# Optimization experiments

Measured on AMD Instinct MI355X. Metric: run time of the kernel, lower is better.

Reference implementation:

```python
import jax, jax.numpy as jnp
import numpy as np

K = 3  # Chebyshev order
B, T, N, FIN, HID = 2, 12, 8192, 8, 16


def cheb_basis(L, X, k):
    # X: [B, N, F] -> stacked Chebyshev polynomials T_0..T_{k-1}: [k, B, N, F]
    T0 = X
    T1 = jnp.einsum('nm,bmf->bnf', L, X)
    Ts = [T0, T1]
    for _ in range(k - 2):
        Ts.append(2.0 * jnp.einsum('nm,bmf->bnf', L, Ts[-1]) - Ts[-2])
    return jnp.stack(Ts)


def setup_inputs() -> dict:
    key = jax.random.key(0)
    ks = jax.random.split(key, 6)
    X = jax.random.normal(ks[0], (B, T, N, FIN), jnp.float32)
    # scaled so spectral radius ~1, like a rescaled Laplacian (keeps Cheb recursion stable)
    L = jax.random.normal(ks[1], (N, N), jnp.float32) * np.float32(1.0 / np.sqrt(N))
    H = jnp.zeros((T, B, N, HID), jnp.float32)
    C = jnp.zeros((T, B, N, HID), jnp.float32)
    sx = np.float32(1.0 / np.sqrt(FIN * K))
    sh = np.float32(1.0 / np.sqrt(HID * K))
    # per-timestep GConvLSTMCore weights; gate order [i, f, c, o]
    Wx = jax.random.normal(ks[2], (T, 4, K, FIN, HID), jnp.float32) * sx
    Wh = jax.random.normal(ks[3], (T, 4, K, HID, HID), jnp.float32) * sh
    bx = jnp.zeros((T, 4, HID), jnp.float32)
    bh = jnp.zeros((T, 4, HID), jnp.float32)
    # peephole weights, order [w_c_i, w_c_f, w_c_o] (glorot init)
    wc = jax.random.normal(ks[4], (T, 3, HID), jnp.float32) * np.float32(0.3)
    # gate biases [b_i, b_f, b_c, b_o] (zeros init per _set_parameters)
    bg = jnp.zeros((T, 4, HID), jnp.float32)
    return dict(X=X, L=L, H=H, C=C, Wx=Wx, Wh=Wh, bx=bx, bh=bh, wc=wc, bg=bg)


def reference(X, L, H, C, Wx, Wh, bx, bh, wc, bg):
    # GConvLSTMCell forward (dropout=0 / eval): per-timestep GConvLSTMCore with its own weights.
    h0, c0 = H[0], C[0]
    Xt = jnp.transpose(X, (1, 0, 2, 3))  # [T, B, N, FIN]

    def step(carry, xs):
        h, c = carry
        x_t, Wx_t, Wh_t, bx_t, bh_t, wc_t, bg_t = xs
        Tx = cheb_basis(L, x_t, K)           # [K, B, N, FIN]
        Th = cheb_basis(L, h, K)             # [K, B, N, HID]
        # fused 4-gate ChebConv: conv_x_*(X,L) + conv_h_*(H,L) incl. conv biases
        pre = (jnp.einsum('kbnf,gkfh->gbnh', Tx, Wx_t) + bx_t[:, None, None, :]
               + jnp.einsum('kbnf,gkfh->gbnh', Th, Wh_t) + bh_t[:, None, None, :])
        i = jax.nn.sigmoid(pre[0] + wc_t[0] * c + bg_t[0])
        f = jax.nn.sigmoid(pre[1] + wc_t[1] * c + bg_t[1])
        c_new = f * c + i * jnp.tanh(pre[2] + bg_t[2])
        o = jax.nn.sigmoid(pre[3] + wc_t[2] * c_new + bg_t[3])  # uses UPDATED cell state
        h_new = o * jnp.tanh(c_new)
        return (h_new, c_new), (h_new, c_new)

    (_, _), (hs, cs) = jax.lax.scan(step, (h0, c0), (Xt, Wx, Wh, bx, bh, wc, bg))
    out = jnp.transpose(hs, (1, 0, 2, 3))  # [B, T, N, HID]
    return out, hs, cs
```

## Files before the change

kernel.cpp:

```cpp
#include <hip/hip_runtime.h>
#include <hip/hip_bf16.h>

#define N_ 8192
#define T_ 12
#define B_ 2
#define FIN_ 8
#define HID_ 16
#define CGSZ 131072

typedef short s8v __attribute__((ext_vector_type(8)));
typedef float f4v __attribute__((ext_vector_type(4)));

__device__ __forceinline__ float sigmoidf_(float x){ return 1.f/(1.f + __expf(-x)); }

__global__ __launch_bounds__(256) void build_Lp_kernel(const float* __restrict__ L,
                                                       __hip_bfloat16* __restrict__ Lp){
  __shared__ unsigned short tile[16][264];
  const int cb = blockIdx.x;
  const int rt = blockIdx.y;
  const int tid = threadIdx.x;
  #pragma unroll
  for (int i = 0; i < 4; ++i){
    int flat = i*256 + tid;
    int r  = flat >> 6;
    int c4 = flat & 63;
    float4 v = *(const float4*)(L + (long)(rt*16 + r)*N_ + cb*256 + c4*4);
    tile[r][c4*4+0] = __bfloat16_as_ushort(__float2bfloat16(v.x));
    tile[r][c4*4+1] = __bfloat16_as_ushort(__float2bfloat16(v.y));
    tile[r][c4*4+2] = __bfloat16_as_ushort(__float2bfloat16(v.z));
    tile[r][c4*4+3] = __bfloat16_as_ushort(__float2bfloat16(v.w));
  }
  __syncthreads();
  #pragma unroll
  for (int j = 0; j < 2; ++j){
    int flat = j*256 + tid;
    int kbl = flat >> 6;
    int l   = flat & 63;
    int lid = l & 15, g = l >> 4;
    uint4 frag = *(const uint4*)&tile[lid][kbl*32 + g*8];
    *(uint4*)(Lp + (((long)rt*256 + cb*8 + kbl)*64 + l)*8) = frag;
  }
}

__global__ __launch_bounds__(256) void pack_xh_kernel(const float* __restrict__ X,
                                                      const float* __restrict__ H,
                                                      __hip_bfloat16* __restrict__ XTf,
                                                      __hip_bfloat16* __restrict__ hTf){
  if (blockIdx.x < 768){
    const int t = blockIdx.x >> 6;
    int flat = (blockIdx.x & 63)*256 + threadIdx.x;
    int l = flat & 63, kb = flat >> 6;
    int lid = l & 15, g = l >> 4;
    int b = lid >> 3, f = lid & 7;
    int n0 = kb*32 + g*8;
    unsigned short u[8];
    #pragma unroll
    for (int e = 0; e < 8; ++e)
      u[e] = __bfloat16_as_ushort(__float2bfloat16(
          X[(((long)(b*T_ + t))*N_ + n0 + e)*FIN_ + f]));
    *(uint4*)(XTf + ((long)t*CGSZ + ((long)kb*64 + l)*8)) = *(uint4*)u;
  } else {
    int flat = (blockIdx.x - 768)*256 + threadIdx.x;
    int l = flat & 63, kb = (flat >> 6) & 255, b = flat >> 14;
    int lid = l & 15, g = l >> 4;
    int n0 = kb*32 + g*8;
    unsigned short u[8];
    #pragma unroll
    for (int e = 0; e < 8; ++e)
      u[e] = __bfloat16_as_ushort(__float2bfloat16(
          H[((long)b*N_ + n0 + e)*HID_ + lid]));
    *(uint4*)(hTf + ((long)b*CGSZ + ((long)kb*64 + l)*8)) = *(uint4*)u;
  }
}

__device__ __forceinline__ void mm_core32(
    const __hip_bfloat16* __restrict__ Lp,
    const __hip_bfloat16* __restrict__ B0f,
    const __hip_bfloat16* __restrict__ B1f,
    const __hip_bfloat16* __restrict__ B2f,
    float (*red)[2][3][64][4], int blk, int w, int lane)
{
  const int kb0 = w*32;
  const s8v* A0 = (const s8v*)(const void*)Lp + ((long)(blk*2+0)*256 + kb0)*64 + lane;
  const s8v* A1 = (const s8v*)(const void*)Lp + ((long)(blk*2+1)*256 + kb0)*64 + lane;
  const s8v* P0 = (const s8v*)(const void*)B0f + (long)kb0*64 + lane;
  const s8v* P1 = (const s8v*)(const void*)B1f + (long)kb0*64 + lane;
  const s8v* P2 = (const s8v*)(const void*)B2f + (long)kb0*64 + lane;
  f4v a00={0.f,0.f,0.f,0.f}, a01={0.f,0.f,0.f,0.f}, a02={0.f,0.f,0.f,0.f};
  f4v a10={0.f,0.f,0.f,0.f}, a11={0.f,0.f,0.f,0.f}, a12={0.f,0.f,0.f,0.f};
  #pragma unroll 8
  for (int kk = 0; kk < 32; ++kk){
    s8v a0 = __builtin_nontemporal_load(A0 + (long)kk*64);
    s8v a1 = __builtin_nontemporal_load(A1 + (long)kk*64);
    s8v b0 = P0[(long)kk*64];
    s8v b1 = P1[(long)kk*64];
    s8v b2 = P2[(long)kk*64];
    a00 = __builtin_amdgcn_mfma_f32_16x16x32_bf16(a0,b0,a00,0,0,0);
    a01 = __builtin_amdgcn_mfma_f32_16x16x32_bf16(a0,b1,a01,0,0,0);
    a02 = __builtin_amdgcn_mfma_f32_16x16x32_bf16(a0,b2,a02,0,0,0);
    a10 = __builtin_amdgcn_mfma_f32_16x16x32_bf16(a1,b0,a10,0,0,0);
    a11 = __builtin_amdgcn_mfma_f32_16x16x32_bf16(a1,b1,a11,0,0,0);
    a12 = __builtin_amdgcn_mfma_f32_16x16x32_bf16(a1,b2,a12,0,0,0);
  }
  *(f4v*)&red[w][0][0][lane][0] = a00;
  *(f4v*)&red[w][0][1][lane][0] = a01;
  *(f4v*)&red[w][0][2][lane][0] = a02;
  *(f4v*)&red[w][1][0][lane][0] = a10;
  *(f4v*)&red[w][1][1][lane][0] = a11;
  *(f4v*)&red[w][1][2][lane][0] = a12;
}

__global__ __launch_bounds__(512) void mm_pass1_kernel(
    const __hip_bfloat16* __restrict__ Lp,
    const __hip_bfloat16* __restrict__ hTf,
    const __hip_bfloat16* __restrict__ XTft,
    __hip_bfloat16* __restrict__ y1f,
    float* __restrict__ u_, float* __restrict__ p_)
{
  __shared__ float red[8][2][3][64][4];
  const int tid = threadIdx.x, w = tid >> 6, lane = tid & 63, blk = blockIdx.x;
  mm_core32(Lp, hTf, hTf + CGSZ, XTft, red, blk, w, lane);
  __syncthreads();
  for (int v = tid; v < 1536; v += 512){
    int rtl = (v >= 768) ? 1 : 0;
    int rem = v - rtl*768;
    int cgI = rem >> 8, r255 = rem & 255;
    int lid = r255 & 15, r = r255 >> 4;
    int g = r >> 2, j = r & 3;
    float s = 0.f;
    #pragma unroll
    for (int ww = 0; ww < 8; ++ww) s += red[ww][rtl][cgI][g*16 + lid][j];
    int n = blk*32 + rtl*16 + r;
    long o = (((long)cgI*256 + (n>>5))*64 + ((n>>3)&3)*16 + lid)*8 + (n&7);
    y1f[o] = __float2bfloat16(s);
    if (cgI < 2) u_[((long)cgI*N_ + n)*HID_ + lid] = s;
    else         p_[((long)(lid>>3)*N_ + n)*FIN_ + (lid&7)] = s;
  }
}

__global__ __launch_bounds__(512) void mm_pass2_gate_kernel(
    const __hip_bfloat16* __restrict__ Lp,
    const __hip_bfloat16* __restrict__ y1f,
    const float* __restrict__ X,
    const float* __restrict__ H0, const float* __restrict__ C0,
    const float* __restrict__ Wx, const float* __restrict__ Wh,
    const float* __restrict__ bx, const float* __restrict__ bh,
    const float* __restrict__ wc, const float* __restrict__ bg,
    const float* __restrict__ u_, const float* __restrict__ p_,
    float* __restrict__ out, float* __restrict__ hs, float* __restrict__ cs,
    __hip_bfloat16* __restrict__ hTf, int t)
{
  __shared__ float red[8][2][3][64][4];
  __shared__ float uv[48][32];
  __shared__ float wlds[4848];
  const int tid = threadIdx.x, w = tid >> 6, lane = tid & 63, blk = blockIdx.x;
  mm_core32(Lp, y1f, y1f + CGSZ, y1f + 2*CGSZ, red, blk, w, lane);
  for (int i = tid; i < 1536; i += 512) wlds[i] = Wx[(long)t*1536 + i];
  for (int i = tid; i < 3072; i += 512) wlds[1536 + i] = Wh[(long)t*3072 + i];
  if (tid < 64){
    wlds[4608 + tid] = bx[t*64 + tid];
    wlds[4672 + tid] = bh[t*64 + tid];
    wlds[4736 + tid] = bg[t*64 + tid];
  }
  if (tid < 48) wlds[4800 + tid] = wc[t*48 + tid];
  __syncthreads();
  for (int v = tid; v < 1536; v += 512){
    int rtl = (v >= 768) ? 1 : 0;
    int rem = v - rtl*768;
    int cgI = rem >> 8, r255 = rem & 255;
    int lid = r255 & 15, r = r255 >> 4;
    int g = r >> 2, j = r & 3;
    float s = 0.f;
    #pragma unroll
    for (int ww = 0; ww < 8; ++ww) s += red[ww][rtl][cgI][g*16 + lid][j];
    uv[cgI*16 + lid][rtl*16 + r] = s;
  }
  __syncthreads();

  #pragma unroll
  for (int it = 0; it < 2; ++it){
    int item = it*512 + tid;
    int gb = item >> 9, rr = (item >> 4) & 31, gh = item & 15;
    int n_g = blk*32 + rr;
    const float* xp = X + (((long)(gb*T_ + t))*N_ + n_g)*FIN_;
    const float* hp = (t==0) ? (H0 + ((long)gb*N_ + n_g)*HID_)
                             : (hs + (((long)(t-1)*B_ + gb)*N_ + n_g)*HID_);
    const float* cp = (t==0) ? (C0 + ((long)gb*N_ + n_g)*HID_)
                             : (cs + (((long)(t-1)*B_ + gb)*N_ + n_g)*HID_);
    const float* up = u_ + ((long)gb*N_ + n_g)*HID_;
    const float* pp = p_ + ((long)gb*N_ + n_g)*FIN_;

    float pre0 = wlds[4608 +  0 + gh] + wlds[4672 +  0 + gh] + wlds[4736 +  0 + gh];
    float pre1 = wlds[4608 + 16 + gh] + wlds[4672 + 16 + gh] + wlds[4736 + 16 + gh];
    float pre2 = wlds[4608 + 32 + gh] + wlds[4672 + 32 + gh] + wlds[4736 + 32 + gh];
    float pre3 = wlds[4608 + 48 + gh] + wlds[4672 + 48 + gh] + wlds[4736 + 48 + gh];
    #pragma unroll
    for (int f = 0; f < 8; ++f){
      float t0 = xp[f];
      float t1 = pp[f];
      float t2 = 2.f*uv[32 + gb*8 + f][rr] - t0;
      pre0 += t0*wlds[((0*3+0)*8+f)*16+gh] + t1*wlds[((0*3+1)*8+f)*16+gh] + t2*wlds[((0*3+2)*8+f)*16+gh];
      pre1 += t0*wlds[((1*3+0)*8+f)*16+gh] + t1*wlds[((1*3+1)*8+f)*16+gh] + t2*wlds[((1*3+2)*8+f)*16+gh];
      pre2 += t0*wlds[((2*3+0)*8+f)*16+gh] + t1*wlds[((2*3+1)*8+f)*16+gh] + t2*wlds[((2*3+2)*8+f)*16+gh];
      pre3 += t0*wlds[((3*3+0)*8+f)*16+gh] + t1*wlds[((3*3+1)*8+f)*16+gh] + t2*wlds[((3*3+2)*8+f)*16+gh];
    }
    #pragma unroll
    for (int j = 0; j < 16; ++j){
      float t0 = hp[j];
      float t1 = up[j];
      float t2 = 2.f*uv[gb*16 + j][rr] - t0;
      pre0 += t0*wlds[1536+((0*3+0)*16+j)*16+gh] + t1*wlds[1536+((0*3+1)*16+j)*16+gh] + t2*wlds[1536+((0*3+2)*16+j)*16+gh];
      pre1 += t0*wlds[1536+((1*3+0)*16+j)*16+gh] + t1*wlds[1536+((1*3+1)*16+j)*16+gh] + t2*wlds[1536+((1*3+2)*16+j)*16+gh];
      pre2 += t0*wlds[1536+((2*3+0)*16+j)*16+gh] + t1*wlds[1536+((2*3+1)*16+j)*16+gh] + t2*wlds[1536+((2*3+2)*16+j)*16+gh];
      pre3 += t0*wlds[1536+((3*3+0)*16+j)*16+gh] + t1*wlds[1536+((3*3+1)*16+j)*16+gh] + t2*wlds[1536+((3*3+2)*16+j)*16+gh];
    }
    float cc = cp[gh];
    float ig = sigmoidf_(pre0 + wlds[4800 +  0 + gh]*cc);
    float fg = sigmoidf_(pre1 + wlds[4800 + 16 + gh]*cc);
    float cnew = fg*cc + ig*tanhf(pre2);
    float og = sigmoidf_(pre3 + wlds[4800 + 32 + gh]*cnew);
    float hn = og*tanhf(cnew);
    hs [(((long)t*B_ + gb)*N_ + n_g)*HID_ + gh] = hn;
    cs [(((long)t*B_ + gb)*N_ + n_g)*HID_ + gh] = cnew;
    out[(((long)gb*T_ + t)*N_ + n_g)*HID_ + gh] = hn;
    const int kb = n_g >> 5, gg = (n_g >> 3) & 3, e = n_g & 7;
    hTf[(((long)gb*256 + kb)*64 + gg*16 + gh)*8 + e] = __float2bfloat16(hn);
  }
}

extern "C" void kernel_launch(void* const* d_in, const int* in_sizes, int n_in,
                              void* d_out, int out_size, void* d_ws, size_t ws_size,
                              hipStream_t stream)
{
  const float* X  = (const float*)d_in[0];
  const float* L  = (const float*)d_in[1];
  const float* H  = (const float*)d_in[2];
  const float* C  = (const float*)d_in[3];
  const float* Wx = (const float*)d_in[4];
  const float* Wh = (const float*)d_in[5];
  const float* bx = (const float*)d_in[6];
  const float* bh = (const float*)d_in[7];
  const float* wc = (const float*)d_in[8];
  const float* bg = (const float*)d_in[9];

  float* out = (float*)d_out;
  float* hs  = out + (long)B_*T_*N_*HID_;
  float* cs  = hs  + (long)T_*B_*N_*HID_;

  const size_t NEEDED = 140247040;
  if (ws_size < NEEDED) return;
  char* ws = (char*)d_ws;
  __hip_bfloat16* Lp  = (__hip_bfloat16*)(ws);
  __hip_bfloat16* XTf = (__hip_bfloat16*)(ws + 134217728);
  __hip_bfloat16* hTf = (__hip_bfloat16*)(ws + 137363456);
  __hip_bfloat16* y1f = (__hip_bfloat16*)(ws + 137887744);
  float* u_ = (float*)(ws + 138674176);
  float* p_ = (float*)(ws + 139722752);

  build_Lp_kernel<<<dim3(32,512), 256, 0, stream>>>(L, Lp);
  pack_xh_kernel <<<896, 256, 0, stream>>>(X, H, XTf, hTf);

  for (int t = 0; t < T_; ++t){
    mm_pass1_kernel<<<256, 512, 0, stream>>>(Lp, hTf, XTf + (long)t*CGSZ,
                                             y1f, u_, p_);
    mm_pass2_gate_kernel<<<256, 512, 0, stream>>>(Lp, y1f, X, H, C,
                                                  Wx, Wh, bx, bh, wc, bg,
                                                  u_, p_, out, hs, cs, hTf, t);
  }
}
```

Measured before the change: 1.271 ms.

## Stream MFMA operands through LDS ring via async global_load_lds prefetch

Replaces the direct global-to-register operand loads in the two Laplacian matmul kernels with a per-wave 3-stage LDS ring buffer filled by global_load_lds. Manual vmcnt and lgkmcnt waits keep three k-steps in flight. The ring's LDS is then reused for the cross-wave reduction, replacing the separate red buffer. The aim is to hide global memory latency behind MFMA work. In exchange, LDS round trips and hand-written waitcnt sequencing are added, and the waits depend on the compiler not emitting other vector memory ops in the loop; the wlds stores issued just before the ring loads are an example of such traffic.

```diff
diff --git a/kernel.cpp b/kernel.cpp
--- a/kernel.cpp
+++ b/kernel.cpp
@@ -12,6 +12,12 @@
 typedef float f4v __attribute__((ext_vector_type(4)));
 
 __device__ __forceinline__ float sigmoidf_(float x){ return 1.f/(1.f + __expf(-x)); }
+
+#define MFMA16(a,b,c) __builtin_amdgcn_mfma_f32_16x16x32_bf16(a,b,c,0,0,0)
+
+#define GLDS16(gsrc, ldst) \
+  __builtin_amdgcn_global_load_lds((const __attribute__((address_space(1))) void*)(gsrc), \
+                                   (__attribute__((address_space(3))) void*)(ldst), 16, 0, 0)
 
 __global__ __launch_bounds__(256) void build_Lp_kernel(const float* __restrict__ L,
                                                        __hip_bfloat16* __restrict__ Lp){
@@ -73,42 +79,60 @@
   }
 }
 
-__device__ __forceinline__ void mm_core32(
-    const __hip_bfloat16* __restrict__ Lp,
-    const __hip_bfloat16* __restrict__ B0f,
-    const __hip_bfloat16* __restrict__ B1f,
-    const __hip_bfloat16* __restrict__ B2f,
-    float (*red)[2][3][64][4], int blk, int w, int lane)
-{
-  const int kb0 = w*32;
-  const s8v* A0 = (const s8v*)(const void*)Lp + ((long)(blk*2+0)*256 + kb0)*64 + lane;
-  const s8v* A1 = (const s8v*)(const void*)Lp + ((long)(blk*2+1)*256 + kb0)*64 + lane;
-  const s8v* P0 = (const s8v*)(const void*)B0f + (long)kb0*64 + lane;
-  const s8v* P1 = (const s8v*)(const void*)B1f + (long)kb0*64 + lane;
-  const s8v* P2 = (const s8v*)(const void*)B2f + (long)kb0*64 + lane;
-  f4v a00={0.f,0.f,0.f,0.f}, a01={0.f,0.f,0.f,0.f}, a02={0.f,0.f,0.f,0.f};
-  f4v a10={0.f,0.f,0.f,0.f}, a11={0.f,0.f,0.f,0.f}, a12={0.f,0.f,0.f,0.f};
-  #pragma unroll 8
-  for (int kk = 0; kk < 32; ++kk){
-    s8v a0 = __builtin_nontemporal_load(A0 + (long)kk*64);
-    s8v a1 = __builtin_nontemporal_load(A1 + (long)kk*64);
-    s8v b0 = P0[(long)kk*64];
-    s8v b1 = P1[(long)kk*64];
-    s8v b2 = P2[(long)kk*64];
-    a00 = __builtin_amdgcn_mfma_f32_16x16x32_bf16(a0,b0,a00,0,0,0);
-    a01 = __builtin_amdgcn_mfma_f32_16x16x32_bf16(a0,b1,a01,0,0,0);
-    a02 = __builtin_amdgcn_mfma_f32_16x16x32_bf16(a0,b2,a02,0,0,0);
-    a10 = __builtin_amdgcn_mfma_f32_16x16x32_bf16(a1,b0,a10,0,0,0);
-    a11 = __builtin_amdgcn_mfma_f32_16x16x32_bf16(a1,b1,a11,0,0,0);
-    a12 = __builtin_amdgcn_mfma_f32_16x16x32_bf16(a1,b2,a12,0,0,0);
-  }
-  *(f4v*)&red[w][0][0][lane][0] = a00;
-  *(f4v*)&red[w][0][1][lane][0] = a01;
-  *(f4v*)&red[w][0][2][lane][0] = a02;
-  *(f4v*)&red[w][1][0][lane][0] = a10;
-  *(f4v*)&red[w][1][1][lane][0] = a11;
-  *(f4v*)&red[w][1][2][lane][0] = a12;
-}
+#define MM_RING_CORE(RING, A0p, A1p, P0p, P1p, P2p)                              \
+  f4v a00={0,0,0,0}, a01={0,0,0,0}, a02={0,0,0,0};                               \
+  f4v a10={0,0,0,0}, a11={0,0,0,0}, a12={0,0,0,0};                               \
+  _Pragma("unroll")                                                              \
+  for (int s = 0; s < 3; ++s){                                                   \
+    GLDS16(A0p + (long)s*64, &RING[w][s][0][0]);                                 \
+    GLDS16(A1p + (long)s*64, &RING[w][s][1][0]);                                 \
+    GLDS16(P0p + (long)s*64, &RING[w][s][2][0]);                                 \
+    GLDS16(P1p + (long)s*64, &RING[w][s][3][0]);                                 \
+    GLDS16(P2p + (long)s*64, &RING[w][s][4][0]);                                 \
+  }                                                                              \
+  _Pragma("unroll")                                                              \
+  for (int kk = 0; kk < 29; ++kk){                                               \
+    const int s = kk % 3;                                                        \
+    asm volatile("s_waitcnt vmcnt(10)" ::: "memory");                            \
+    s8v a0 = RING[w][s][0][lane];                                                \
+    s8v a1 = RING[w][s][1][lane];                                                \
+    s8v b0 = RING[w][s][2][lane];                                                \
+    s8v b1 = RING[w][s][3][lane];                                                \
+    s8v b2 = RING[w][s][4][lane];                                                \
+    asm volatile("s_waitcnt lgkmcnt(0)" ::: "memory");                           \
+    GLDS16(A0p + (long)(kk+3)*64, &RING[w][s][0][0]);                            \
+    GLDS16(A1p + (long)(kk+3)*64, &RING[w][s][1][0]);                            \
+    GLDS16(P0p + (long)(kk+3)*64, &RING[w][s][2][0]);                            \
+    GLDS16(P1p + (long)(kk+3)*64, &RING[w][s][3][0]);                            \
+    GLDS16(P2p + (long)(kk+3)*64, &RING[w][s][4][0]);                            \
+    a00 = MFMA16(a0,b0,a00); a01 = MFMA16(a0,b1,a01); a02 = MFMA16(a0,b2,a02);   \
+    a10 = MFMA16(a1,b0,a10); a11 = MFMA16(a1,b1,a11); a12 = MFMA16(a1,b2,a12);   \
+  }                                                                              \
+  _Pragma("unroll")                                                              \
+  for (int kk = 29; kk < 32; ++kk){                                              \
+    const int s = kk % 3;                                                        \
+    if (kk == 29) { asm volatile("s_waitcnt vmcnt(10)" ::: "memory"); }          \
+    else if (kk == 30) { asm volatile("s_waitcnt vmcnt(5)" ::: "memory"); }      \
+    else { asm volatile("s_waitcnt vmcnt(0)" ::: "memory"); }                    \
+    s8v a0 = RING[w][s][0][lane];                                                \
+    s8v a1 = RING[w][s][1][lane];                                                \
+    s8v b0 = RING[w][s][2][lane];                                                \
+    s8v b1 = RING[w][s][3][lane];                                                \
+    s8v b2 = RING[w][s][4][lane];                                                \
+    asm volatile("s_waitcnt lgkmcnt(0)" ::: "memory");                           \
+    a00 = MFMA16(a0,b0,a00); a01 = MFMA16(a0,b1,a01); a02 = MFMA16(a0,b2,a02);   \
+    a10 = MFMA16(a1,b0,a10); a11 = MFMA16(a1,b1,a11); a12 = MFMA16(a1,b2,a12);   \
+  }                                                                              \
+    \
+  {                                                                              \
+    float* rw = (float*)&RING[w][0][0][0];                                       \
+    *(f4v*)&rw[((0*3+0)*64 + lane)*4] = a00;                                     \
+    *(f4v*)&rw[((0*3+1)*64 + lane)*4] = a01;                                     \
+    *(f4v*)&rw[((0*3+2)*64 + lane)*4] = a02;                                     \
+    *(f4v*)&rw[((1*3+0)*64 + lane)*4] = a10;                                     \
+    *(f4v*)&rw[((1*3+1)*64 + lane)*4] = a11;                                     \
+    *(f4v*)&rw[((1*3+2)*64 + lane)*4] = a12;                                     \
+  }
 
 __global__ __launch_bounds__(512) void mm_pass1_kernel(
     const __hip_bfloat16* __restrict__ Lp,
@@ -117,9 +141,17 @@
     __hip_bfloat16* __restrict__ y1f,
     float* __restrict__ u_, float* __restrict__ p_)
 {
-  __shared__ float red[8][2][3][64][4];
+  __shared__ s8v ring[8][3][5][64];
   const int tid = threadIdx.x, w = tid >> 6, lane = tid & 63, blk = blockIdx.x;
-  mm_core32(Lp, hTf, hTf + CGSZ, XTft, red, blk, w, lane);
+  const int kb0 = w*32;
+  const s8v* A0p = (const s8v*)(const void*)Lp + ((long)(blk*2+0)*256 + kb0)*64 + lane;
+  const s8v* A1p = (const s8v*)(const void*)Lp + ((long)(blk*2+1)*256 + kb0)*64 + lane;
+  const s8v* P0p = (const s8v*)(const void*)hTf + (long)kb0*64 + lane;
+  const s8v* P1p = (const s8v*)(const void*)(hTf + CGSZ) + (long)kb0*64 + lane;
+  const s8v* P2p = (const s8v*)(const void*)XTft + (long)kb0*64 + lane;
+
+  MM_RING_CORE(ring, A0p, A1p, P0p, P1p, P2p)
+
   __syncthreads();
   for (int v = tid; v < 1536; v += 512){
     int rtl = (v >= 768) ? 1 : 0;
@@ -129,7 +161,10 @@
     int g = r >> 2, j = r & 3;
     float s = 0.f;
     #pragma unroll
-    for (int ww = 0; ww < 8; ++ww) s += red[ww][rtl][cgI][g*16 + lid][j];
+    for (int ww = 0; ww < 8; ++ww){
+      const float* rw = (const float*)&ring[ww][0][0][0];
+      s += rw[((rtl*3 + cgI)*64 + g*16 + lid)*4 + j];
+    }
     int n = blk*32 + rtl*16 + r;
     long o = (((long)cgI*256 + (n>>5))*64 + ((n>>3)&3)*16 + lid)*8 + (n&7);
     y1f[o] = __float2bfloat16(s);
@@ -150,11 +185,11 @@
     float* __restrict__ out, float* __restrict__ hs, float* __restrict__ cs,
     __hip_bfloat16* __restrict__ hTf, int t)
 {
-  __shared__ float red[8][2][3][64][4];
+  __shared__ s8v ring[8][3][5][64];
   __shared__ float uv[48][32];
   __shared__ float wlds[4848];
   const int tid = threadIdx.x, w = tid >> 6, lane = tid & 63, blk = blockIdx.x;
-  mm_core32(Lp, y1f, y1f + CGSZ, y1f + 2*CGSZ, red, blk, w, lane);
+
   for (int i = tid; i < 1536; i += 512) wlds[i] = Wx[(long)t*1536 + i];
   for (int i = tid; i < 3072; i += 512) wlds[1536 + i] = Wh[(long)t*3072 + i];
   if (tid < 64){
@@ -163,6 +198,16 @@
     wlds[4736 + tid] = bg[t*64 + tid];
   }
   if (tid < 48) wlds[4800 + tid] = wc[t*48 + tid];
+
+  const int kb0 = w*32;
+  const s8v* A0p = (const s8v*)(const void*)Lp + ((long)(blk*2+0)*256 + kb0)*64 + lane;
+  const s8v* A1p = (const s8v*)(const void*)Lp + ((long)(blk*2+1)*256 + kb0)*64 + lane;
+  const s8v* P0p = (const s8v*)(const void*)y1f + (long)kb0*64 + lane;
+  const s8v* P1p = (const s8v*)(const void*)(y1f + CGSZ) + (long)kb0*64 + lane;
+  const s8v* P2p = (const s8v*)(const void*)(y1f + 2*CGSZ) + (long)kb0*64 + lane;
+
+  MM_RING_CORE(ring, A0p, A1p, P0p, P1p, P2p)
+
   __syncthreads();
   for (int v = tid; v < 1536; v += 512){
     int rtl = (v >= 768) ? 1 : 0;
@@ -172,7 +217,10 @@
     int g = r >> 2, j = r & 3;
     float s = 0.f;
     #pragma unroll
-    for (int ww = 0; ww < 8; ++ww) s += red[ww][rtl][cgI][g*16 + lid][j];
+    for (int ww = 0; ww < 8; ++ww){
+      const float* rw = (const float*)&ring[ww][0][0][0];
+      s += rw[((rtl*3 + cgI)*64 + g*16 + lid)*4 + j];
+    }
     uv[cgI*16 + lid][rtl*16 + r] = s;
   }
   __syncthreads();
```

Measured after the change: 1.150 ms. 9.5% less time.

## Software-pipeline MFMA matmul core with inline-asm buffer loads and explicit vmcnt waits

Applied to the files above, without the earlier changes.

Replaces the compiler-scheduled global loads in the L-times-basis MFMA core with inline-asm buffer_load_dwordx4 instructions. They use buffer resource descriptors and a three-stage register ring, with explicit s_waitcnt vmcnt so that loads stay about three k-steps ahead of the MFMAs. The A (Laplacian) stream uses the sc1 cache hint in place of nontemporal loads. In the gate kernel, the weight staging into LDS now runs before the matmul, which may let those loads overlap. This adds register pressure and relies on hand-counted vmcnt values and manually built descriptors, which is fragile.

```diff
diff --git a/kernel.cpp b/kernel.cpp
--- a/kernel.cpp
+++ b/kernel.cpp
@@ -10,8 +10,30 @@
 
 typedef short s8v __attribute__((ext_vector_type(8)));
 typedef float f4v __attribute__((ext_vector_type(4)));
+typedef unsigned u32x4 __attribute__((ext_vector_type(4)));
 
 __device__ __forceinline__ float sigmoidf_(float x){ return 1.f/(1.f + __expf(-x)); }
+
+#define MFMA16(a,b,c) __builtin_amdgcn_mfma_f32_16x16x32_bf16(a,b,c,0,0,0)
+
+__device__ __forceinline__ u32x4 make_srsrc(const void* p, unsigned bytes){
+  unsigned long a = (unsigned long)p;
+  u32x4 r;
+  r.x = (unsigned)a;
+  r.y = (unsigned)(a >> 32) & 0xFFFFu;
+  r.z = bytes;
+  r.w = 0x00020000u;
+  return r;
+}
+
+#define BLOAD_A(dst, rsrc, voff) \
+  asm volatile("buffer_load_dwordx4 %0, %1, %2, 0 offen sc1" \
+               : "=v"(dst) : "v"(voff), "s"(rsrc) : "memory")
+#define BLOAD_B(dst, rsrc, voff) \
+  asm volatile("buffer_load_dwordx4 %0, %1, %2, 0 offen" \
+               : "=v"(dst) : "v"(voff), "s"(rsrc) : "memory")
+#define WAITV(n) do { asm volatile("s_waitcnt vmcnt(" #n ")" ::: "memory"); \
+                      __builtin_amdgcn_sched_barrier(0); } while(0)
 
 __global__ __launch_bounds__(256) void build_Lp_kernel(const float* __restrict__ L,
                                                        __hip_bfloat16* __restrict__ Lp){
@@ -73,42 +95,41 @@
   }
 }
 
-__device__ __forceinline__ void mm_core32(
-    const __hip_bfloat16* __restrict__ Lp,
-    const __hip_bfloat16* __restrict__ B0f,
-    const __hip_bfloat16* __restrict__ B1f,
-    const __hip_bfloat16* __restrict__ B2f,
-    float (*red)[2][3][64][4], int blk, int w, int lane)
-{
-  const int kb0 = w*32;
-  const s8v* A0 = (const s8v*)(const void*)Lp + ((long)(blk*2+0)*256 + kb0)*64 + lane;
-  const s8v* A1 = (const s8v*)(const void*)Lp + ((long)(blk*2+1)*256 + kb0)*64 + lane;
-  const s8v* P0 = (const s8v*)(const void*)B0f + (long)kb0*64 + lane;
-  const s8v* P1 = (const s8v*)(const void*)B1f + (long)kb0*64 + lane;
-  const s8v* P2 = (const s8v*)(const void*)B2f + (long)kb0*64 + lane;
-  f4v a00={0.f,0.f,0.f,0.f}, a01={0.f,0.f,0.f,0.f}, a02={0.f,0.f,0.f,0.f};
-  f4v a10={0.f,0.f,0.f,0.f}, a11={0.f,0.f,0.f,0.f}, a12={0.f,0.f,0.f,0.f};
-  #pragma unroll 8
-  for (int kk = 0; kk < 32; ++kk){
-    s8v a0 = __builtin_nontemporal_load(A0 + (long)kk*64);
-    s8v a1 = __builtin_nontemporal_load(A1 + (long)kk*64);
-    s8v b0 = P0[(long)kk*64];
-    s8v b1 = P1[(long)kk*64];
-    s8v b2 = P2[(long)kk*64];
-    a00 = __builtin_amdgcn_mfma_f32_16x16x32_bf16(a0,b0,a00,0,0,0);
-    a01 = __builtin_amdgcn_mfma_f32_16x16x32_bf16(a0,b1,a01,0,0,0);
-    a02 = __builtin_amdgcn_mfma_f32_16x16x32_bf16(a0,b2,a02,0,0,0);
-    a10 = __builtin_amdgcn_mfma_f32_16x16x32_bf16(a1,b0,a10,0,0,0);
-    a11 = __builtin_amdgcn_mfma_f32_16x16x32_bf16(a1,b1,a11,0,0,0);
-    a12 = __builtin_amdgcn_mfma_f32_16x16x32_bf16(a1,b2,a12,0,0,0);
-  }
-  *(f4v*)&red[w][0][0][lane][0] = a00;
-  *(f4v*)&red[w][0][1][lane][0] = a01;
-  *(f4v*)&red[w][0][2][lane][0] = a02;
-  *(f4v*)&red[w][1][0][lane][0] = a10;
-  *(f4v*)&red[w][1][1][lane][0] = a11;
+#define MM_ASM_CORE(rsA, voffA0_, voffA1_, rsB0, rsB1, rsB2, voffB_)             \
+  f4v a00={0,0,0,0}, a01={0,0,0,0}, a02={0,0,0,0};                               \
+  f4v a10={0,0,0,0}, a11={0,0,0,0}, a12={0,0,0,0};                               \
+  s8v rA0[3], rA1[3], rB0[3], rB1[3], rB2[3];                                    \
+  _Pragma("unroll")                                                              \
+  for (int s = 0; s < 3; ++s){                                                   \
+    BLOAD_A(rA0[s], rsA,  voffA0_ + s*1024u);                                    \
+    BLOAD_A(rA1[s], rsA,  voffA1_ + s*1024u);                                    \
+    BLOAD_B(rB0[s], rsB0, voffB_  + s*1024u);                                    \
+    BLOAD_B(rB1[s], rsB1, voffB_  + s*1024u);                                    \
+    BLOAD_B(rB2[s], rsB2, voffB_  + s*1024u);                                    \
+  }                                                                              \
+  _Pragma("unroll")                                                              \
+  for (int kk = 0; kk < 32; ++kk){                                               \
+    const int s = kk % 3;                                                        \
+    if (kk < 30)      WAITV(10);                                                 \
+    else if (kk == 30) WAITV(5);                                                 \
+    else               WAITV(0);                                                 \
+    s8v a0 = rA0[s], a1 = rA1[s], b0 = rB0[s], b1 = rB1[s], b2 = rB2[s];         \
+    if (kk < 29){                                                                \
+      BLOAD_A(rA0[s], rsA,  voffA0_ + (kk+3)*1024u);                             \
+      BLOAD_A(rA1[s], rsA,  voffA1_ + (kk+3)*1024u);                             \
+      BLOAD_B(rB0[s], rsB0, voffB_  + (kk+3)*1024u);                             \
+      BLOAD_B(rB1[s], rsB1, voffB_  + (kk+3)*1024u);                             \
+      BLOAD_B(rB2[s], rsB2, voffB_  + (kk+3)*1024u);                             \
+    }                                                                            \
+    a00 = MFMA16(a0,b0,a00); a01 = MFMA16(a0,b1,a01); a02 = MFMA16(a0,b2,a02);   \
+    a10 = MFMA16(a1,b0,a10); a11 = MFMA16(a1,b1,a11); a12 = MFMA16(a1,b2,a12);   \
+  }                                                                              \
+  *(f4v*)&red[w][0][0][lane][0] = a00;                                           \
+  *(f4v*)&red[w][0][1][lane][0] = a01;                                           \
+  *(f4v*)&red[w][0][2][lane][0] = a02;                                           \
+  *(f4v*)&red[w][1][0][lane][0] = a10;                                           \
+  *(f4v*)&red[w][1][1][lane][0] = a11;                                           \
   *(f4v*)&red[w][1][2][lane][0] = a12;
-}
 
 __global__ __launch_bounds__(512) void mm_pass1_kernel(
     const __hip_bfloat16* __restrict__ Lp,
@@ -119,7 +140,18 @@
 {
   __shared__ float red[8][2][3][64][4];
   const int tid = threadIdx.x, w = tid >> 6, lane = tid & 63, blk = blockIdx.x;
-  mm_core32(Lp, hTf, hTf + CGSZ, XTft, red, blk, w, lane);
+  const int kb0 = w*32;
+
+  const u32x4 rsA  = make_srsrc(Lp, 134217728u);
+  const u32x4 rsB0 = make_srsrc(hTf, 262144u);
+  const u32x4 rsB1 = make_srsrc(hTf + CGSZ, 262144u);
+  const u32x4 rsB2 = make_srsrc(XTft, 262144u);
+  const unsigned voffA0 = (unsigned)((((blk*2+0)*256 + kb0)*64 + lane)*16);
+  const unsigned voffA1 = (unsigned)((((blk*2+1)*256 + kb0)*64 + lane)*16);
+  const unsigned voffB  = (unsigned)(((kb0)*64 + lane)*16);
+
+  MM_ASM_CORE(rsA, voffA0, voffA1, rsB0, rsB1, rsB2, voffB)
+
   __syncthreads();
   for (int v = tid; v < 1536; v += 512){
     int rtl = (v >= 768) ? 1 : 0;
@@ -154,7 +186,7 @@
   __shared__ float uv[48][32];
   __shared__ float wlds[4848];
   const int tid = threadIdx.x, w = tid >> 6, lane = tid & 63, blk = blockIdx.x;
-  mm_core32(Lp, y1f, y1f + CGSZ, y1f + 2*CGSZ, red, blk, w, lane);
+
   for (int i = tid; i < 1536; i += 512) wlds[i] = Wx[(long)t*1536 + i];
   for (int i = tid; i < 3072; i += 512) wlds[1536 + i] = Wh[(long)t*3072 + i];
   if (tid < 64){
@@ -163,6 +195,19 @@
     wlds[4736 + tid] = bg[t*64 + tid];
   }
   if (tid < 48) wlds[4800 + tid] = wc[t*48 + tid];
+  __builtin_amdgcn_sched_barrier(0);
+
+  const int kb0 = w*32;
+  const u32x4 rsA  = make_srsrc(Lp, 134217728u);
+  const u32x4 rsB0 = make_srsrc(y1f, 262144u);
+  const u32x4 rsB1 = make_srsrc(y1f + CGSZ, 262144u);
+  const u32x4 rsB2 = make_srsrc(y1f + 2*CGSZ, 262144u);
+  const unsigned voffA0 = (unsigned)((((blk*2+0)*256 + kb0)*64 + lane)*16);
+  const unsigned voffA1 = (unsigned)((((blk*2+1)*256 + kb0)*64 + lane)*16);
+  const unsigned voffB  = (unsigned)(((kb0)*64 + lane)*16);
+
+  MM_ASM_CORE(rsA, voffA0, voffA1, rsB0, rsB1, rsB2, voffB)
+
   __syncthreads();
   for (int v = tid; v < 1536; v += 512){
     int rtl = (v >= 768) ? 1 : 0;
```

Result: faster. 1.097 ms, median of 2 (-13.6%).
